# Kernel tuning notes

Measured on AMD Instinct MI355X. Metric: run time of the kernel, lower is better.

## Reference

```python
import jax, jax.numpy as jnp
import numpy as np


def setup_inputs() -> dict:
    key = jax.random.key(0)
    ks = jax.random.split(key, 5)
    S, B, I, H = 512, 64, 512, 512
    scale_in = 1.0 / np.sqrt(I)
    scale_h = 1.0 / np.sqrt(H)
    return {
        "x": jax.random.normal(ks[0], (S, B, I), dtype=jnp.float32),
        "W1": jax.random.normal(ks[1], (H, I), dtype=jnp.float32) * scale_in,
        "b1": jax.random.normal(ks[2], (H,), dtype=jnp.float32) * scale_in,
        "W2": jax.random.normal(ks[3], (H, H), dtype=jnp.float32) * scale_h,
        "b2": jax.random.normal(ks[4], (H,), dtype=jnp.float32) * scale_h,
    }


def reference(x, W1, b1, W2, b2):
    # Elman RNN: h_t = tanh(x_t @ W1^T + b1 + h_{t-1} @ W2^T + b2)
    # Precompute the input projection for all timesteps in one big GEMM.
    # x: [S, B, I] -> xp: [S, B, H]
    xp = jnp.einsum('sbi,hi->sbh', x, W1) + b1
    B, H = x.shape[1], W2.shape[0]
    h0 = jnp.zeros((B, H), dtype=x.dtype)

    def step(h, xp_t):
        h_new = jnp.tanh(xp_t + h @ W2.T + b2)
        return h_new, h_new

    h_last, h_seq = jax.lax.scan(step, h0, xp)
    return h_seq, h_last
```

## Files before the change

kernel.cpp:

```cpp
#include <hip/hip_runtime.h>
#include <math.h>

#define SS 512
#define BB 64
#define II 512
#define HH 512
#define MM (SS*BB)

typedef _Float16 h2 __attribute__((ext_vector_type(2)));
typedef _Float16 f16x8 __attribute__((ext_vector_type(8)));
typedef float f32x4 __attribute__((ext_vector_type(4)));

__device__ __forceinline__ h2 bc_h2(unsigned u) { return __builtin_bit_cast(h2, u); }
__device__ __forceinline__ unsigned bc_u(h2 v) { return __builtin_bit_cast(unsigned, v); }
__device__ __forceinline__ h2 pk(float x, float y) {
    return __builtin_bit_cast(h2, __builtin_amdgcn_cvt_pkrtz(x, y));
}

#if __has_builtin(__builtin_amdgcn_exp2f)
#define EXP2F __builtin_amdgcn_exp2f
#else
#define EXP2F exp2f
#endif
#if __has_builtin(__builtin_amdgcn_rcpf)
#define RCPF __builtin_amdgcn_rcpf
#else
#define RCPF(x) (1.0f / (x))
#endif

__device__ __forceinline__ float fast_tanh(float z) {
    float e = EXP2F(z * 2.885390081777927f);
    return 1.0f - 2.0f * RCPF(e + 1.0f);
}

__device__ __forceinline__ void bar_lds() {
    asm volatile("s_waitcnt lgkmcnt(0)\n\ts_barrier" ::: "memory");
}

__global__ __launch_bounds__(256) void k_ingemm2(const float* __restrict__ X,
                                                 const float* __restrict__ W1,
                                                 const float* __restrict__ b1,
                                                 float* __restrict__ C) {
    __shared__ __align__(16) _Float16 As[128 * 32];
    __shared__ __align__(16) _Float16 Bs[128 * 32];
    const int bm = blockIdx.x * 128;
    const int bn = blockIdx.y * 128;
    const int t = threadIdx.x;
    const int lane = t & 63;
    const int w = t >> 6;
    const int srow = t >> 1;
    const int kb0 = (t & 1) * 32;
    const int wm = (w >> 1) * 64, wn = (w & 1) * 64;

    f32x4 acc[4][4];
#pragma unroll
    for (int i = 0; i < 4; i++)
#pragma unroll
        for (int j = 0; j < 4; j++) acc[i][j] = f32x4{0.f, 0.f, 0.f, 0.f};

    const float* xs = X + (size_t)(bm + srow) * II + (t & 1) * 16;
    const float* ws = W1 + (size_t)(bn + srow) * II + (t & 1) * 16;
    char* asb = (char*)As + srow * 64;
    char* bsb = (char*)Bs + srow * 64;
    const int sw = (srow & 3) << 4;

    const int frow = lane & 15;
    const int fkb = (lane >> 4) * 16;
    const int fsw = (frow & 3) << 4;

    for (int kt = 0; kt < 16; ++kt) {
        float4 a0 = *(const float4*)(xs + kt * 32 + 0);
        float4 a1 = *(const float4*)(xs + kt * 32 + 4);
        float4 a2 = *(const float4*)(xs + kt * 32 + 8);
        float4 a3 = *(const float4*)(xs + kt * 32 + 12);
        float4 c0 = *(const float4*)(ws + kt * 32 + 0);
        float4 c1 = *(const float4*)(ws + kt * 32 + 4);
        float4 c2 = *(const float4*)(ws + kt * 32 + 8);
        float4 c3 = *(const float4*)(ws + kt * 32 + 12);
        __syncthreads();
        uint4 u0, u1, v0, v1;
        u0.x = bc_u(pk(a0.x, a0.y)); u0.y = bc_u(pk(a0.z, a0.w));
        u0.z = bc_u(pk(a1.x, a1.y)); u0.w = bc_u(pk(a1.z, a1.w));
        u1.x = bc_u(pk(a2.x, a2.y)); u1.y = bc_u(pk(a2.z, a2.w));
        u1.z = bc_u(pk(a3.x, a3.y)); u1.w = bc_u(pk(a3.z, a3.w));
        v0.x = bc_u(pk(c0.x, c0.y)); v0.y = bc_u(pk(c0.z, c0.w));
        v0.z = bc_u(pk(c1.x, c1.y)); v0.w = bc_u(pk(c1.z, c1.w));
        v1.x = bc_u(pk(c2.x, c2.y)); v1.y = bc_u(pk(c2.z, c2.w));
        v1.z = bc_u(pk(c3.x, c3.y)); v1.w = bc_u(pk(c3.z, c3.w));
        *(uint4*)(asb + ((kb0 + 0) ^ sw)) = u0;
        *(uint4*)(asb + ((kb0 + 16) ^ sw)) = u1;
        *(uint4*)(bsb + ((kb0 + 0) ^ sw)) = v0;
        *(uint4*)(bsb + ((kb0 + 16) ^ sw)) = v1;
        __syncthreads();

        f16x8 af[4], bf[4];
#pragma unroll
        for (int i = 0; i < 4; i++) {
            const int ar = wm + 16 * i + frow;
            af[i] = *(const f16x8*)((const char*)As + ar * 64 + (fkb ^ fsw));
            const int br = wn + 16 * i + frow;
            bf[i] = *(const f16x8*)((const char*)Bs + br * 64 + (fkb ^ fsw));
        }
#pragma unroll
        for (int i = 0; i < 4; i++)
#pragma unroll
            for (int j = 0; j < 4; j++)
                acc[i][j] = __builtin_amdgcn_mfma_f32_16x16x32_f16(
                    af[i], bf[j], acc[i][j], 0, 0, 0);
    }

    const int erow = bm + wm + (lane >> 4) * 4;
    const int ecol = bn + wn + (lane & 15);
#pragma unroll
    for (int j = 0; j < 4; j++) {
        const float bj = b1[ecol + 16 * j];
#pragma unroll
        for (int i = 0; i < 4; i++)
#pragma unroll
            for (int r = 0; r < 4; r++)
                C[(size_t)(erow + 16 * i + r) * HH + ecol + 16 * j] =
                    acc[i][j][r] + bj;
    }
}

__global__ __attribute__((amdgpu_flat_work_group_size(512, 512)))
__attribute__((amdgpu_waves_per_eu(2, 2)))
void k_rec8(const float* __restrict__ W2,
            const float* __restrict__ b2,
            float* __restrict__ out,
            float* __restrict__ hlast) {
    const int b = blockIdx.x;
    const int t = threadIdx.x;
    const int lane = t & 63;
    const int w = t >> 6;

    __shared__ uint4 wlds[16][512];
    __shared__ float part[8][512];
    __shared__ __align__(4) _Float16 hsmem[HH];
    const unsigned* hs32 = (const unsigned*)hsmem;

    h2 wreg[6][32];
#pragma unroll
    for (int ci = 0; ci < 6; ci++) {
        const float2* src =
            (const float2*)(W2 + (size_t)(lane + 64 * ci) * HH) + (w << 5);
#pragma unroll
        for (int g = 0; g < 32; g++) wreg[ci][g] = pk(src[g].x, src[g].y);
    }
#pragma unroll
    for (int cc = 0; cc < 2; cc++) {
        const float2* src =
            (const float2*)(W2 + (size_t)(lane + 384 + 64 * cc) * HH) + (w << 5);
#pragma unroll
        for (int q = 0; q < 8; q++) {
            uint4 u;
            u.x = bc_u(pk(src[4 * q + 0].x, src[4 * q + 0].y));
            u.y = bc_u(pk(src[4 * q + 1].x, src[4 * q + 1].y));
            u.z = bc_u(pk(src[4 * q + 2].x, src[4 * q + 2].y));
            u.w = bc_u(pk(src[4 * q + 3].x, src[4 * q + 3].y));
            wlds[cc * 8 + q][t] = u;
        }
    }
    hsmem[t] = (_Float16)0.0f;
    const float bias = b2[t];
    float* po = out + (size_t)b * HH + t;
    float hn = 0.0f;
    __syncthreads();

    for (int step = 0; step < SS; ++step) {
        float xpv = *po;
        unsigned hv = hs32[(w << 5) + (lane & 31)];

        h2 accA[8], accB[8];
#pragma unroll
        for (int c = 0; c < 8; c++) { accA[c] = h2{0, 0}; accB[c] = h2{0, 0}; }

#pragma unroll
        for (int q = 0; q < 8; q++) {
            uint4 u6 = wlds[q][t];
            uint4 u7 = wlds[8 + q][t];
            unsigned w6[4] = {u6.x, u6.y, u6.z, u6.w};
            unsigned w7[4] = {u7.x, u7.y, u7.z, u7.w};
#pragma unroll
            for (int gg = 0; gg < 4; gg++) {
                const int g = 4 * q + gg;
                h2 hp = bc_h2((unsigned)__builtin_amdgcn_readlane((int)hv, g));
                if (gg & 1) {
                    accB[0] += wreg[0][g] * hp;
                    accB[1] += wreg[1][g] * hp;
                    accB[2] += wreg[2][g] * hp;
                    accB[3] += wreg[3][g] * hp;
                    accB[4] += wreg[4][g] * hp;
                    accB[5] += wreg[5][g] * hp;
                    accB[6] += bc_h2(w6[gg]) * hp;
                    accB[7] += bc_h2(w7[gg]) * hp;
                } else {
                    accA[0] += wreg[0][g] * hp;
                    accA[1] += wreg[1][g] * hp;
                    accA[2] += wreg[2][g] * hp;
                    accA[3] += wreg[3][g] * hp;
                    accA[4] += wreg[4][g] * hp;
                    accA[5] += wreg[5][g] * hp;
                    accA[6] += bc_h2(w6[gg]) * hp;
                    accA[7] += bc_h2(w7[gg]) * hp;
                }
            }
        }
#pragma unroll
        for (int c = 0; c < 8; c++) {
            h2 s = accA[c] + accB[c];
            part[w][lane + 64 * c] = (float)s.x + (float)s.y;
        }
        bar_lds();

        float z = part[0][t] + part[1][t] + part[2][t] + part[3][t] +
                  part[4][t] + part[5][t] + part[6][t] + part[7][t] +
                  bias + xpv;
        hn = fast_tanh(z);
        hsmem[t] = (_Float16)hn;
        *po = hn;
        po += BB * HH;
        bar_lds();
    }
    hlast[(size_t)b * HH + t] = hn;
}

extern "C" void kernel_launch(void* const* d_in, const int* in_sizes, int n_in,
                              void* d_out, int out_size, void* d_ws, size_t ws_size,
                              hipStream_t stream) {
    const float* x  = (const float*)d_in[0];
    const float* W1 = (const float*)d_in[1];
    const float* b1 = (const float*)d_in[2];
    const float* W2 = (const float*)d_in[3];
    const float* b2 = (const float*)d_in[4];
    float* out = (float*)d_out;

    k_ingemm2<<<dim3(MM / 128, HH / 128), 256, 0, stream>>>(x, W1, b1, out);
    k_rec8<<<BB, 512, 0, stream>>>(W2, b2, out, out + (size_t)SS * BB * HH);
}
```

Before: 875.8 us.

## Split each batch recurrence across two workgroups exchanging hidden halves via global flags

Adds k_rec9, which splits each batch element's recurrence across two workgroups (128 total). Each workgroup owns half of the hidden columns and keeps all of its W2 slice in registers, so the LDS-resident weights are no longer needed. The two halves swap packed fp16 hidden values every step through a workspace buffer, using atomic stores and a spin-wait on a 0xFFFFFFFF sentinel set by a memset. This doubles parallelism and halves per-step FMA work, but puts a cross-CU global-memory handshake on the critical path of every step and relies on both workgroups being co-resident.

```diff
diff --git a/kernel.cpp b/kernel.cpp
--- a/kernel.cpp
+++ b/kernel.cpp
@@ -6,6 +6,8 @@
 #define II 512
 #define HH 512
 #define MM (SS*BB)
+#define HXC_WORDS ((size_t)SS * BB * 256)
+#define HXC_BYTES (HXC_WORDS * 4)
 
 typedef _Float16 h2 __attribute__((ext_vector_type(2)));
 typedef _Float16 f16x8 __attribute__((ext_vector_type(8)));
@@ -125,6 +127,121 @@
 
 __global__ __attribute__((amdgpu_flat_work_group_size(512, 512)))
 __attribute__((amdgpu_waves_per_eu(2, 2)))
+void k_rec9(const float* __restrict__ W2,
+            const float* __restrict__ b2,
+            float* __restrict__ out,
+            float* __restrict__ hlast,
+            unsigned* __restrict__ hxc) {
+    const int wgid = blockIdx.x;
+    const int b = wgid & 63;
+    const int half = wgid >> 6;
+    const int t = threadIdx.x;
+    const int lane = t & 63;
+    const int wv = t >> 6;
+    const int colbase = half << 8;
+
+    __shared__ float part[8][256];
+    __shared__ __align__(4) _Float16 hsmem[256];
+    const unsigned* hs32 = (const unsigned*)hsmem;
+
+    h2 wreg[4][32];
+    {
+        const int pown = (half << 7) + (wv << 4);
+        const int popp = ((1 - half) << 7) + (wv << 4);
+#pragma unroll
+        for (int ci = 0; ci < 4; ci++) {
+            const float2* wrow =
+                (const float2*)(W2 + (size_t)(colbase + lane + (ci << 6)) * HH);
+#pragma unroll
+            for (int g = 0; g < 16; g++) {
+                float2 f = wrow[pown + g];
+                wreg[ci][g] = pk(f.x, f.y);
+            }
+#pragma unroll
+            for (int g = 0; g < 16; g++) {
+                float2 f = wrow[popp + g];
+                wreg[ci][16 + g] = pk(f.x, f.y);
+            }
+        }
+    }
+    if (t < 256) hsmem[t] = (_Float16)0.0f;
+    float bias = 0.f;
+    if (t < 256) bias = b2[colbase + t];
+    float* po = out + (size_t)b * HH + colbase + t;
+    const unsigned* rd = hxc + (size_t)b * 256 + ((1 - half) << 7) +
+                         (wv << 4) + (lane & 15);
+    unsigned* wr = hxc + (size_t)b * 256 + (half << 7) + (t >> 1);
+    float hn = 0.0f;
+    __syncthreads();
+
+    for (int s = 0; s < SS; ++s) {
+        float xpv = 0.f;
+        if (t < 256) xpv = *po;
+
+        unsigned hv1 = hs32[(wv << 4) + (lane & 15)];
+        h2 aA[4], aB[4];
+#pragma unroll
+        for (int ci = 0; ci < 4; ci++) { aA[ci] = h2{0, 0}; aB[ci] = h2{0, 0}; }
+#pragma unroll
+        for (int g = 0; g < 16; g++) {
+            h2 hp = bc_h2((unsigned)__builtin_amdgcn_readlane((int)hv1, g));
+            if (g & 1) {
+                aB[0] += wreg[0][g] * hp; aB[1] += wreg[1][g] * hp;
+                aB[2] += wreg[2][g] * hp; aB[3] += wreg[3][g] * hp;
+            } else {
+                aA[0] += wreg[0][g] * hp; aA[1] += wreg[1][g] * hp;
+                aA[2] += wreg[2][g] * hp; aA[3] += wreg[3][g] * hp;
+            }
+        }
+
+        unsigned hv2 = 0;
+        if (s > 0) {
+            const unsigned* p = rd + (size_t)(s - 1) * (BB * 256);
+            do {
+                hv2 = __hip_atomic_load(p, __ATOMIC_RELAXED,
+                                        __HIP_MEMORY_SCOPE_AGENT);
+            } while (hv2 == 0xFFFFFFFFu);
+        }
+#pragma unroll
+        for (int g = 0; g < 16; g++) {
+            h2 hp = bc_h2((unsigned)__builtin_amdgcn_readlane((int)hv2, g));
+            if (g & 1) {
+                aB[0] += wreg[0][16 + g] * hp; aB[1] += wreg[1][16 + g] * hp;
+                aB[2] += wreg[2][16 + g] * hp; aB[3] += wreg[3][16 + g] * hp;
+            } else {
+                aA[0] += wreg[0][16 + g] * hp; aA[1] += wreg[1][16 + g] * hp;
+                aA[2] += wreg[2][16 + g] * hp; aA[3] += wreg[3][16 + g] * hp;
+            }
+        }
+#pragma unroll
+        for (int ci = 0; ci < 4; ci++) {
+            h2 sv = aA[ci] + aB[ci];
+            part[wv][lane + (ci << 6)] = (float)sv.x + (float)sv.y;
+        }
+        bar_lds();
+
+        if (t < 256) {
+            float z = part[0][t] + part[1][t] + part[2][t] + part[3][t] +
+                      part[4][t] + part[5][t] + part[6][t] + part[7][t] +
+                      bias + xpv;
+            hn = fast_tanh(z);
+            *po = hn;
+            hsmem[t] = (_Float16)hn;
+            float ho = __shfl_xor(hn, 1);
+            if (!(t & 1)) {
+                __hip_atomic_store(wr + (size_t)s * (BB * 256),
+                                   bc_u(pk(hn, ho)),
+                                   __ATOMIC_RELAXED, __HIP_MEMORY_SCOPE_AGENT);
+            }
+        }
+        po += BB * HH;
+        bar_lds();
+    }
+    if (t < 256) hlast[(size_t)b * HH + colbase + t] = hn;
+}
+
+__global__ __attribute__((amdgpu_flat_work_group_size(512, 512)))
+__attribute__((amdgpu_waves_per_eu(2, 2)))
 void k_rec8(const float* __restrict__ W2,
             const float* __restrict__ b2,
             float* __restrict__ out,
@@ -174,7 +291,6 @@
         h2 accA[8], accB[8];
 #pragma unroll
         for (int c = 0; c < 8; c++) { accA[c] = h2{0, 0}; accB[c] = h2{0, 0}; }
-
 #pragma unroll
         for (int q = 0; q < 8; q++) {
             uint4 u6 = wlds[q][t];
@@ -186,21 +302,15 @@
                 const int g = 4 * q + gg;
                 h2 hp = bc_h2((unsigned)__builtin_amdgcn_readlane((int)hv, g));
                 if (gg & 1) {
-                    accB[0] += wreg[0][g] * hp;
-                    accB[1] += wreg[1][g] * hp;
-                    accB[2] += wreg[2][g] * hp;
-                    accB[3] += wreg[3][g] * hp;
-                    accB[4] += wreg[4][g] * hp;
-                    accB[5] += wreg[5][g] * hp;
+                    accB[0] += wreg[0][g] * hp; accB[1] += wreg[1][g] * hp;
+                    accB[2] += wreg[2][g] * hp; accB[3] += wreg[3][g] * hp;
+                    accB[4] += wreg[4][g] * hp; accB[5] += wreg[5][g] * hp;
                     accB[6] += bc_h2(w6[gg]) * hp;
                     accB[7] += bc_h2(w7[gg]) * hp;
                 } else {
-                    accA[0] += wreg[0][g] * hp;
-                    accA[1] += wreg[1][g] * hp;
-                    accA[2] += wreg[2][g] * hp;
-                    accA[3] += wreg[3][g] * hp;
-                    accA[4] += wreg[4][g] * hp;
-                    accA[5] += wreg[5][g] * hp;
+                    accA[0] += wreg[0][g] * hp; accA[1] += wreg[1][g] * hp;
+                    accA[2] += wreg[2][g] * hp; accA[3] += wreg[3][g] * hp;
+                    accA[4] += wreg[4][g] * hp; accA[5] += wreg[5][g] * hp;
                     accA[6] += bc_h2(w6[gg]) * hp;
                     accA[7] += bc_h2(w7[gg]) * hp;
                 }
@@ -236,5 +346,12 @@
     float* out = (float*)d_out;
 
     k_ingemm2<<<dim3(MM / 128, HH / 128), 256, 0, stream>>>(x, W1, b1, out);
-    k_rec8<<<BB, 512, 0, stream>>>(W2, b2, out, out + (size_t)SS * BB * HH);
-}
+    if (ws_size >= HXC_BYTES) {
+        unsigned* hxc = (unsigned*)d_ws;
+        hipMemsetAsync(d_ws, 0xFF, HXC_BYTES, stream);
+        k_rec9<<<128, 512, 0, stream>>>(W2, b2, out,
+                                        out + (size_t)SS * BB * HH, hxc);
+    } else {
+        k_rec8<<<BB, 512, 0, stream>>>(W2, b2, out, out + (size_t)SS * BB * HH);
+    }
+}
```

Measured after the change: 711.3 us, median of 2. 1.23x faster.
